# Kernel optimization log

Measured on AMD Instinct MI355X. Metric: run time of the kernel, lower is better.

Reference implementation:

```python
import jax, jax.numpy as jnp
import numpy as np

N_HARMONICS = 128
N_STEPS = 1024
N_SAMPLES = 262144


def setup_inputs() -> dict:
    key = jax.random.key(0)
    k1, k2 = jax.random.split(key)
    scores = jax.random.uniform(k1, (N_SAMPLES,), dtype=jnp.float32)  # scores assumed in [0,1]
    targets = jax.random.bernoulli(k2, 0.5, (N_SAMPLES,))
    return {"scores": scores, "targets": targets}


def _chain_fourier(s_basis, c_basis, mask, two_pi_k):
    """compute_fourier + normalize_by_samples + integrate (termwise) for one class.

    s_basis/c_basis: (K, N) precomputed sin/cos(2*pi*k*s); mask: (N,) float 0/1.
    Masked sum == ragged nonzero+gather in the original, same math.
    """
    eps = jnp.finfo(jnp.float32).eps
    n = jnp.sum(mask)
    safe_n = jnp.maximum(n, eps)
    # _norm_or_pass: zero coefficients if the class is empty, else divide by count
    sin_c = jnp.where(n < eps, 0.0, (s_basis @ mask) / safe_n)  # (K,)
    cos_c = jnp.where(n < eps, 0.0, (c_basis @ mask) / safe_n)
    # termwise integration of sum_k [sin_c sin(wx) + cos_c cos(wx)], w = 2*pi*k:
    # int sin(wx) dx = -cos(wx)/w ; int cos(wx) dx = sin(wx)/w
    int_sin = cos_c / two_pi_k
    int_cos = -sin_c / two_pi_k
    return int_sin, int_cos


def _normalized_cdf(thrs, sin_c, cos_c, two_pi_k):
    # evaluate_fourier on n_steps thresholds, then normalize_cdf: [1, 1-0.5*(cdf+0.5), 0]
    ang = thrs[:, None] * two_pi_k[None, :]  # (S, K)
    cdf = jnp.sin(ang) @ sin_c + jnp.cos(ang) @ cos_c  # (S,)
    one = jnp.ones((1,), dtype=cdf.dtype)
    zero = jnp.zeros((1,), dtype=cdf.dtype)
    return jnp.concatenate([one, 1.0 - 0.5 * (cdf + 0.5), zero])


def reference(scores, targets):
    two_pi_k = 2.0 * jnp.pi * jnp.arange(1, N_HARMONICS + 1, dtype=jnp.float32)  # (K,)
    ang = two_pi_k[:, None] * scores[None, :]  # (K, N) dominant intermediate
    s_basis = jnp.sin(ang)
    c_basis = jnp.cos(ang)
    pos_mask = targets.astype(jnp.float32)
    neg_mask = 1.0 - pos_mask
    ps, pc = _chain_fourier(s_basis, c_basis, pos_mask, two_pi_k)
    ns, nc = _chain_fourier(s_basis, c_basis, neg_mask, two_pi_k)
    thrs = jnp.linspace(0.0, 1.0, N_STEPS, dtype=jnp.float32)
    pos_norm = _normalized_cdf(thrs, ps, pc, two_pi_k)  # (S+2,)
    neg_norm = _normalized_cdf(thrs, ns, nc, two_pi_k)
    # AUC via Riemann integration of one CDF against the other
    pos_auc = jnp.sum(pos_norm[:-1] * (-jnp.diff(neg_norm)))
    neg_auc = 1.0 + jnp.sum(neg_norm[:-1] * jnp.diff(pos_norm))
    # statistic == 'flatten': single column -> flatten scalar to shape (1,)
    return jnp.reshape(0.5 * (pos_auc + neg_auc), (1,))
```

## Files before the change

kernel.cpp:

```cpp
#include <hip/hip_runtime.h>
#include <hip/hip_bf16.h>


#define NK 128
#define NSTEPS 1024
#define K1_TPB 256
#define CHUNK 256
#define REP 8
#define RSTRIDE 520
#define DET_BLOCKS 64
#define DET_TPB 256
#define K2_TPB 1024

__device__ __forceinline__ float wave_sum(float v) {
  #pragma unroll
  for (int off = 32; off > 0; off >>= 1) v += __shfl_down(v, off, 64);
  return v;
}

__device__ __forceinline__ float block_sum(float v, float* scratch) {
  int lane = threadIdx.x & 63, wid = threadIdx.x >> 6;
  v = wave_sum(v);
  if (lane == 0) scratch[wid] = v;
  __syncthreads();
  float r = 0.0f;
  if (threadIdx.x == 0) {
    int nw = blockDim.x >> 6;
    for (int w = 0; w < nw; ++w) r += scratch[w];
  }
  return r;
}

__global__ __launch_bounds__(DET_TPB) void k_detect(const unsigned char* __restrict__ t,
                                                    int nbytes,
                                                    unsigned* __restrict__ flags,
                                                    float* __restrict__ acc) {
  __shared__ unsigned s_or;
  const int gid = blockIdx.x * DET_TPB + threadIdx.x;
  if (threadIdx.x == 0) s_or = 0u;
  for (int i = gid; i < REP * RSTRIDE; i += DET_BLOCKS * DET_TPB) acc[i] = 0.0f;
  __syncthreads();
  unsigned local = 0u;
  int n16 = nbytes >> 4;
  const uint4* p = (const uint4*)t;
  for (int i = gid; i < n16; i += DET_BLOCKS * DET_TPB) {
    uint4 v = p[i];
    local |= v.x | v.y | v.z | v.w;
  }
  if (gid < (nbytes & 15)) {
    int i = (n16 << 4) + gid;
    local |= ((unsigned)t[i]) << ((i & 3) * 8);
  }
  if (local) atomicOr(&s_or, local);
  __syncthreads();
  if (threadIdx.x == 0) flags[blockIdx.x] = s_or;
}

__device__ __forceinline__ int decode_mode(const unsigned* __restrict__ flags) {
  unsigned o = 0u;
  #pragma unroll
  for (int i = 0; i < DET_BLOCKS; ++i) o |= flags[i];
  if (o == 0u) return 0;
  bool nz0 = (o & 0xFFu) != 0u;
  bool nz1 = (o & 0xFF00u) != 0u;
  if (!nz1 && !(o & 0xFFFF0000u)) return 1;
  if (!nz0 && !nz1) return 2;
  return 0;
}

__global__ __launch_bounds__(K1_TPB) void k_partial(const float* __restrict__ scores,
                                                    const unsigned char* __restrict__ tgt,
                                                    int N,
                                                    const unsigned* __restrict__ flags,
                                                    float* __restrict__ acc) {
  __shared__ float2 s_d[CHUNK];
  __shared__ float s_comb[NK * 4];
  __shared__ float s_red[K1_TPB / 64];
  __shared__ int s_mode;
  if (threadIdx.x == 0) s_mode = decode_mode(flags);
  __syncthreads();
  const int mode = s_mode;
  const int base = blockIdx.x * CHUNK;

  float m = 0.0f;
  {
    int g = base + threadIdx.x;
    float s = 0.0f;
    if (g < N) {
      s = scores[g];
      if (mode == 0)      m = (float)tgt[g];
      else if (mode == 1) m = (float)((const int*)tgt)[g];
      else                m = ((const float*)tgt)[g];
    }
    s_d[threadIdx.x] = make_float2(s, m);
  }
  __syncthreads();
  float cnt = block_sum(m, s_red);

  const int k_idx = threadIdx.x & (NK - 1);
  const int half = threadIdx.x >> 7;
  const float kf = (float)(k_idx + 1);
  const int HC = CHUNK / 2;
  const int i0 = half * HC;

  float ps0 = 0.f, pc0 = 0.f, ts0 = 0.f, tc0 = 0.f;
  float ps1 = 0.f, pc1 = 0.f, ts1 = 0.f, tc1 = 0.f;
  for (int i = 0; i < HC; i += 8) {
    float2 r[8];
    #pragma unroll
    for (int j = 0; j < 8; ++j) r[j] = s_d[i0 + i + j];
    #pragma unroll
    for (int j = 0; j < 8; ++j) {
      float x = kf * r[j].x;
      float f = __builtin_amdgcn_fractf(x);
      float sn = __builtin_amdgcn_sinf(f);
      float cs = __builtin_amdgcn_cosf(f);
      if (j & 1) {
        ts1 += sn; tc1 += cs;
        ps1 = fmaf(r[j].y, sn, ps1); pc1 = fmaf(r[j].y, cs, pc1);
      } else {
        ts0 += sn; tc0 += cs;
        ps0 = fmaf(r[j].y, sn, ps0); pc0 = fmaf(r[j].y, cs, pc0);
      }
    }
  }
  float ps = ps0 + ps1, pc = pc0 + pc1, ts = ts0 + ts1, tc = tc0 + tc1;
  int valid = min(max(N - base - i0, 0), HC);
  tc -= (float)(HC - valid);

  if (half == 1) {
    s_comb[k_idx * 4 + 0] = ps;
    s_comb[k_idx * 4 + 1] = pc;
    s_comb[k_idx * 4 + 2] = ts;
    s_comb[k_idx * 4 + 3] = tc;
  }
  __syncthreads();
  float* ab = acc + (size_t)(blockIdx.x & (REP - 1)) * RSTRIDE;
  if (half == 0) {
    atomicAdd(&ab[k_idx * 4 + 0], ps + s_comb[k_idx * 4 + 0]);
    atomicAdd(&ab[k_idx * 4 + 1], pc + s_comb[k_idx * 4 + 1]);
    atomicAdd(&ab[k_idx * 4 + 2], ts + s_comb[k_idx * 4 + 2]);
    atomicAdd(&ab[k_idx * 4 + 3], tc + s_comb[k_idx * 4 + 3]);
  }
  if (threadIdx.x == 0) atomicAdd(&ab[NK * 4], cnt);
}

__global__ __launch_bounds__(K2_TPB) void k_final(const float* __restrict__ acc,
                                                  int N,
                                                  float* __restrict__ out) {
  __shared__ float s_sums[NK * 4];
  __shared__ float s_isp[NK], s_icp[NK], s_isn[NK], s_icn[NK];
  __shared__ float s_pn[NSTEPS + 2], s_nn[NSTEPS + 2];
  __shared__ float s_red[K2_TPB / 64];
  __shared__ float s_npos;
  const int tid = threadIdx.x;

  if (tid < NK * 4) {
    float v = 0.0f;
    #pragma unroll
    for (int r = 0; r < REP; ++r) v += acc[r * RSTRIDE + tid];
    s_sums[tid] = v;
  }
  if (tid == 0) {
    float v = 0.0f;
    #pragma unroll
    for (int r = 0; r < REP; ++r) v += acc[r * RSTRIDE + NK * 4];
    s_npos = v;
  }
  __syncthreads();

  if (tid < NK) {
    const float eps = 1.1920929e-07f;
    float npos = s_npos;
    float nneg = (float)N - npos;
    float sp = s_sums[tid * 4 + 0], cp = s_sums[tid * 4 + 1];
    float st = s_sums[tid * 4 + 2], ct = s_sums[tid * 4 + 3];
    float scp, ccp, scn, ccn;
    if (npos < eps) { scp = 0.0f; ccp = 0.0f; }
    else { float d = fmaxf(npos, eps); scp = sp / d; ccp = cp / d; }
    if (nneg < eps) { scn = 0.0f; ccn = 0.0f; }
    else { float d = fmaxf(nneg, eps); scn = (st - sp) / d; ccn = (ct - cp) / d; }
    float w = 6.2831853071795864769f * (float)(tid + 1);
    s_isp[tid] = ccp / w;  s_icp[tid] = -scp / w;
    s_isn[tid] = ccn / w;  s_icn[tid] = -scn / w;
  }
  __syncthreads();

  {
    float thr = (float)tid * (1.0f / 1023.0f);
    float cp_acc = 0.0f, cn_acc = 0.0f;
    #pragma unroll 4
    for (int k = 0; k < NK; ++k) {
      float x = (float)(k + 1) * thr;
      float f = __builtin_amdgcn_fractf(x);
      float sn = __builtin_amdgcn_sinf(f);
      float cs = __builtin_amdgcn_cosf(f);
      cp_acc += sn * s_isp[k] + cs * s_icp[k];
      cn_acc += sn * s_isn[k] + cs * s_icn[k];
    }
    s_pn[tid + 1] = 1.0f - 0.5f * (cp_acc + 0.5f);
    s_nn[tid + 1] = 1.0f - 0.5f * (cn_acc + 0.5f);
  }
  if (tid == 0) {
    s_pn[0] = 1.0f; s_nn[0] = 1.0f;
    s_pn[NSTEPS + 1] = 0.0f; s_nn[NSTEPS + 1] = 0.0f;
  }
  __syncthreads();

  float pa = 0.0f, na = 0.0f;
  for (int i = tid; i < NSTEPS + 1; i += K2_TPB) {
    float p0 = s_pn[i], p1 = s_pn[i + 1];
    float n0 = s_nn[i], n1 = s_nn[i + 1];
    pa = fmaf(p0, n0 - n1, pa);
    na = fmaf(n0, p1 - p0, na);
  }
  float paS = block_sum(pa, s_red);
  __syncthreads();
  float naS = block_sum(na, s_red);
  if (tid == 0) out[0] = 0.5f * (paS + (1.0f + naS));
}

extern "C" void kernel_launch(void* const* d_in, const int* in_sizes, int n_in,
                              void* d_out, int out_size, void* d_ws, size_t ws_size,
                              hipStream_t stream) {
  const float* scores = (const float*)d_in[0];
  const unsigned char* targets = (const unsigned char*)d_in[1];
  const int N = in_sizes[0];

  unsigned* flags = (unsigned*)d_ws;
  float* acc = (float*)((char*)d_ws + 512);

  const int nblocks = (N + CHUNK - 1) / CHUNK;

  k_detect<<<DET_BLOCKS, DET_TPB, 0, stream>>>(targets, N, flags, acc);
  k_partial<<<nblocks, K1_TPB, 0, stream>>>(scores, targets, N, flags, acc);
  k_final<<<1, K2_TPB, 0, stream>>>(acc, N, (float*)d_out);
}
```

Measured before the change: 93.88 us.

## Fuse final reduction into partial kernel via last-block ticket

Merges the single-block finalization kernel into the main partial-sum kernel. Each block takes an atomic ticket after its atomics, and the last block to arrive reads the accumulators and computes the CDF evaluation and AUC with 256 threads, each handling 4 thresholds. This removes one kernel launch and its gap. In exchange it adds a serialized tail on one block with a quarter as many threads, plus an extra atomic per block and a larger shared-memory footprint per block through a union.

```diff
diff --git a/kernel.cpp b/kernel.cpp
--- a/kernel.cpp
+++ b/kernel.cpp
@@ -8,9 +8,9 @@
 #define CHUNK 256
 #define REP 8
 #define RSTRIDE 520
+#define ZTOT (REP * RSTRIDE + 16)
 #define DET_BLOCKS 64
 #define DET_TPB 256
-#define K2_TPB 1024
 
 __device__ __forceinline__ float wave_sum(float v) {
   #pragma unroll
@@ -38,7 +38,7 @@
   __shared__ unsigned s_or;
   const int gid = blockIdx.x * DET_TPB + threadIdx.x;
   if (threadIdx.x == 0) s_or = 0u;
-  for (int i = gid; i < REP * RSTRIDE; i += DET_BLOCKS * DET_TPB) acc[i] = 0.0f;
+  for (int i = gid; i < ZTOT; i += DET_BLOCKS * DET_TPB) acc[i] = 0.0f;
   __syncthreads();
   unsigned local = 0u;
   int n16 = nbytes >> 4;
@@ -68,23 +68,36 @@
   return 0;
 }
 
-__global__ __launch_bounds__(K1_TPB) void k_partial(const float* __restrict__ scores,
-                                                    const unsigned char* __restrict__ tgt,
-                                                    int N,
-                                                    const unsigned* __restrict__ flags,
-                                                    float* __restrict__ acc) {
-  __shared__ float2 s_d[CHUNK];
-  __shared__ float s_comb[NK * 4];
+union SharedB {
+  struct { float2 d[CHUNK]; float comb[NK * 4]; } p;
+  struct {
+    float sums[NK * 4];
+    float isp[NK], icp[NK], isn[NK], icn[NK];
+    float pn[NSTEPS + 2], nn[NSTEPS + 2];
+    float npos;
+  } f;
+};
+
+__global__ __launch_bounds__(K1_TPB) void k_main(const float* __restrict__ scores,
+                                                 const unsigned char* __restrict__ tgt,
+                                                 int N,
+                                                 const unsigned* __restrict__ flags,
+                                                 float* __restrict__ acc,
+                                                 unsigned* __restrict__ ticket,
+                                                 float* __restrict__ out) {
+  __shared__ SharedB sh;
   __shared__ float s_red[K1_TPB / 64];
   __shared__ int s_mode;
-  if (threadIdx.x == 0) s_mode = decode_mode(flags);
+  __shared__ int s_last;
+  const int tid = threadIdx.x;
+  if (tid == 0) s_mode = decode_mode(flags);
   __syncthreads();
   const int mode = s_mode;
   const int base = blockIdx.x * CHUNK;
 
   float m = 0.0f;
   {
-    int g = base + threadIdx.x;
+    int g = base + tid;
     float s = 0.0f;
     if (g < N) {
       s = scores[g];
@@ -92,13 +105,13 @@
       else if (mode == 1) m = (float)((const int*)tgt)[g];
       else                m = ((const float*)tgt)[g];
     }
-    s_d[threadIdx.x] = make_float2(s, m);
+    sh.p.d[tid] = make_float2(s, m);
   }
   __syncthreads();
   float cnt = block_sum(m, s_red);
 
-  const int k_idx = threadIdx.x & (NK - 1);
-  const int half = threadIdx.x >> 7;
+  const int k_idx = tid & (NK - 1);
+  const int half = tid >> 7;
   const float kf = (float)(k_idx + 1);
   const int HC = CHUNK / 2;
   const int i0 = half * HC;
@@ -108,7 +121,7 @@
   for (int i = 0; i < HC; i += 8) {
     float2 r[8];
     #pragma unroll
-    for (int j = 0; j < 8; ++j) r[j] = s_d[i0 + i + j];
+    for (int j = 0; j < 8; ++j) r[j] = sh.p.d[i0 + i + j];
     #pragma unroll
     for (int j = 0; j < 8; ++j) {
       float x = kf * r[j].x;
@@ -129,88 +142,100 @@
   tc -= (float)(HC - valid);
 
   if (half == 1) {
-    s_comb[k_idx * 4 + 0] = ps;
-    s_comb[k_idx * 4 + 1] = pc;
-    s_comb[k_idx * 4 + 2] = ts;
-    s_comb[k_idx * 4 + 3] = tc;
+    sh.p.comb[k_idx * 4 + 0] = ps;
+    sh.p.comb[k_idx * 4 + 1] = pc;
+    sh.p.comb[k_idx * 4 + 2] = ts;
+    sh.p.comb[k_idx * 4 + 3] = tc;
   }
   __syncthreads();
   float* ab = acc + (size_t)(blockIdx.x & (REP - 1)) * RSTRIDE;
   if (half == 0) {
-    atomicAdd(&ab[k_idx * 4 + 0], ps + s_comb[k_idx * 4 + 0]);
-    atomicAdd(&ab[k_idx * 4 + 1], pc + s_comb[k_idx * 4 + 1]);
-    atomicAdd(&ab[k_idx * 4 + 2], ts + s_comb[k_idx * 4 + 2]);
-    atomicAdd(&ab[k_idx * 4 + 3], tc + s_comb[k_idx * 4 + 3]);
-  }
-  if (threadIdx.x == 0) atomicAdd(&ab[NK * 4], cnt);
-}
-
-__global__ __launch_bounds__(K2_TPB) void k_final(const float* __restrict__ acc,
-                                                  int N,
-                                                  float* __restrict__ out) {
-  __shared__ float s_sums[NK * 4];
-  __shared__ float s_isp[NK], s_icp[NK], s_isn[NK], s_icn[NK];
-  __shared__ float s_pn[NSTEPS + 2], s_nn[NSTEPS + 2];
-  __shared__ float s_red[K2_TPB / 64];
-  __shared__ float s_npos;
-  const int tid = threadIdx.x;
-
-  if (tid < NK * 4) {
+    atomicAdd(&ab[k_idx * 4 + 0], ps + sh.p.comb[k_idx * 4 + 0]);
+    atomicAdd(&ab[k_idx * 4 + 1], pc + sh.p.comb[k_idx * 4 + 1]);
+    atomicAdd(&ab[k_idx * 4 + 2], ts + sh.p.comb[k_idx * 4 + 2]);
+    atomicAdd(&ab[k_idx * 4 + 3], tc + sh.p.comb[k_idx * 4 + 3]);
+  }
+  if (tid == 0) atomicAdd(&ab[NK * 4], cnt);
+
+  __syncthreads();
+  if (tid == 0) {
+    __threadfence();
+    unsigned r = __hip_atomic_fetch_add(ticket, 1u, __ATOMIC_ACQ_REL,
+                                        __HIP_MEMORY_SCOPE_AGENT);
+    s_last = (r == (unsigned)(gridDim.x - 1)) ? 1 : 0;
+  }
+  __syncthreads();
+  if (!s_last) return;
+
+  for (int q = tid; q < NK * 4; q += K1_TPB) {
     float v = 0.0f;
     #pragma unroll
-    for (int r = 0; r < REP; ++r) v += acc[r * RSTRIDE + tid];
-    s_sums[tid] = v;
+    for (int r = 0; r < REP; ++r)
+      v += __hip_atomic_load(&acc[r * RSTRIDE + q], __ATOMIC_RELAXED,
+                             __HIP_MEMORY_SCOPE_AGENT);
+    sh.f.sums[q] = v;
   }
   if (tid == 0) {
     float v = 0.0f;
     #pragma unroll
-    for (int r = 0; r < REP; ++r) v += acc[r * RSTRIDE + NK * 4];
-    s_npos = v;
+    for (int r = 0; r < REP; ++r)
+      v += __hip_atomic_load(&acc[r * RSTRIDE + NK * 4], __ATOMIC_RELAXED,
+                             __HIP_MEMORY_SCOPE_AGENT);
+    sh.f.npos = v;
   }
   __syncthreads();
 
   if (tid < NK) {
     const float eps = 1.1920929e-07f;
-    float npos = s_npos;
+    float npos = sh.f.npos;
     float nneg = (float)N - npos;
-    float sp = s_sums[tid * 4 + 0], cp = s_sums[tid * 4 + 1];
-    float st = s_sums[tid * 4 + 2], ct = s_sums[tid * 4 + 3];
+    float sp = sh.f.sums[tid * 4 + 0], cp = sh.f.sums[tid * 4 + 1];
+    float st = sh.f.sums[tid * 4 + 2], ct = sh.f.sums[tid * 4 + 3];
     float scp, ccp, scn, ccn;
     if (npos < eps) { scp = 0.0f; ccp = 0.0f; }
     else { float d = fmaxf(npos, eps); scp = sp / d; ccp = cp / d; }
     if (nneg < eps) { scn = 0.0f; ccn = 0.0f; }
     else { float d = fmaxf(nneg, eps); scn = (st - sp) / d; ccn = (ct - cp) / d; }
     float w = 6.2831853071795864769f * (float)(tid + 1);
-    s_isp[tid] = ccp / w;  s_icp[tid] = -scp / w;
-    s_isn[tid] = ccn / w;  s_icn[tid] = -scn / w;
+    sh.f.isp[tid] = ccp / w;  sh.f.icp[tid] = -scp / w;
+    sh.f.isn[tid] = ccn / w;  sh.f.icn[tid] = -scn / w;
   }
   __syncthreads();
 
   {
-    float thr = (float)tid * (1.0f / 1023.0f);
-    float cp_acc = 0.0f, cn_acc = 0.0f;
-    #pragma unroll 4
+    float th[4], cp_[4] = {0, 0, 0, 0}, cn_[4] = {0, 0, 0, 0};
+    #pragma unroll
+    for (int q = 0; q < 4; ++q) th[q] = (float)(tid + q * K1_TPB) * (1.0f / 1023.0f);
     for (int k = 0; k < NK; ++k) {
-      float x = (float)(k + 1) * thr;
-      float f = __builtin_amdgcn_fractf(x);
-      float sn = __builtin_amdgcn_sinf(f);
-      float cs = __builtin_amdgcn_cosf(f);
-      cp_acc += sn * s_isp[k] + cs * s_icp[k];
-      cn_acc += sn * s_isn[k] + cs * s_icn[k];
-    }
-    s_pn[tid + 1] = 1.0f - 0.5f * (cp_acc + 0.5f);
-    s_nn[tid + 1] = 1.0f - 0.5f * (cn_acc + 0.5f);
+      float isp = sh.f.isp[k], icp = sh.f.icp[k];
+      float isn = sh.f.isn[k], icn = sh.f.icn[k];
+      float kf1 = (float)(k + 1);
+      #pragma unroll
+      for (int q = 0; q < 4; ++q) {
+        float f = __builtin_amdgcn_fractf(kf1 * th[q]);
+        float sn = __builtin_amdgcn_sinf(f);
+        float cs = __builtin_amdgcn_cosf(f);
+        cp_[q] = fmaf(sn, isp, fmaf(cs, icp, cp_[q]));
+        cn_[q] = fmaf(sn, isn, fmaf(cs, icn, cn_[q]));
+      }
+    }
+    #pragma unroll
+    for (int q = 0; q < 4; ++q) {
+      int t = tid + q * K1_TPB;
+      sh.f.pn[t + 1] = 1.0f - 0.5f * (cp_[q] + 0.5f);
+      sh.f.nn[t + 1] = 1.0f - 0.5f * (cn_[q] + 0.5f);
+    }
   }
   if (tid == 0) {
-    s_pn[0] = 1.0f; s_nn[0] = 1.0f;
-    s_pn[NSTEPS + 1] = 0.0f; s_nn[NSTEPS + 1] = 0.0f;
+    sh.f.pn[0] = 1.0f; sh.f.nn[0] = 1.0f;
+    sh.f.pn[NSTEPS + 1] = 0.0f; sh.f.nn[NSTEPS + 1] = 0.0f;
   }
   __syncthreads();
 
   float pa = 0.0f, na = 0.0f;
-  for (int i = tid; i < NSTEPS + 1; i += K2_TPB) {
-    float p0 = s_pn[i], p1 = s_pn[i + 1];
-    float n0 = s_nn[i], n1 = s_nn[i + 1];
+  for (int i = tid; i < NSTEPS + 1; i += K1_TPB) {
+    float p0 = sh.f.pn[i], p1 = sh.f.pn[i + 1];
+    float n0 = sh.f.nn[i], n1 = sh.f.nn[i + 1];
     pa = fmaf(p0, n0 - n1, pa);
     na = fmaf(n0, p1 - p0, na);
   }
@@ -229,10 +254,11 @@
 
   unsigned* flags = (unsigned*)d_ws;
   float* acc = (float*)((char*)d_ws + 512);
+  unsigned* ticket = (unsigned*)(acc + REP * RSTRIDE);
 
   const int nblocks = (N + CHUNK - 1) / CHUNK;
 
   k_detect<<<DET_BLOCKS, DET_TPB, 0, stream>>>(targets, N, flags, acc);
-  k_partial<<<nblocks, K1_TPB, 0, stream>>>(scores, targets, N, flags, acc);
-  k_final<<<1, K2_TPB, 0, stream>>>(acc, N, (float*)d_out);
-}
+  k_main<<<nblocks, K1_TPB, 0, stream>>>(scores, targets, N, flags, acc, ticket,
+                                         (float*)d_out);
+}
```

After: 107.3 us. 1.14x slower.
